# Performance work log

Hardware: AMD Instinct MI355X
Metric: run time of the kernel (lower is better)

Reference implementation:

```python
import jax, jax.numpy as jnp
import numpy as np

N_KERNELS = 5
MUL_FACTOR = 2.0
# 2.0 ** (arange(5) - 2) = [0.25, 0.5, 1, 2, 4]
BANDWIDTH_MULTIPLIERS = MUL_FACTOR ** (np.arange(N_KERNELS) - N_KERNELS // 2)


def setup_inputs() -> dict:
    key = jax.random.key(0)
    kx, ky = jax.random.split(key)
    X = jax.random.normal(kx, (4096, 256), dtype=jnp.float32)
    Y = jax.random.normal(ky, (4096, 256), dtype=jnp.float32)
    return {"X": X, "Y": Y}


def _pairwise_sq_dists(Z):
    # ||z_i - z_j||^2 via GEMM; clamp tiny negatives from roundoff.
    sq = jnp.sum(Z * Z, axis=-1)  # [2N]
    d2 = sq[:, None] + sq[None, :] - 2.0 * (Z @ Z.T)  # [2N, 2N]
    return jnp.maximum(d2, 0.0)


def reference(X, Y):
    n = X.shape[0]
    Z = jnp.concatenate([X, Y], axis=0)  # [2N, D]
    d2 = _pairwise_sq_dists(Z)  # [2N, 2N]
    n_samples = d2.shape[0]
    # bandwidth uses .data in torch -> detached
    bandwidth = jax.lax.stop_gradient(d2.sum()) / (n_samples ** 2 - n_samples)
    mults = jnp.asarray(BANDWIDTH_MULTIPLIERS, dtype=d2.dtype)  # [5]
    # K = sum_k exp(-d2 / (bandwidth * mult_k))
    K = jnp.exp(-d2[None, :, :] / (bandwidth * mults)[:, None, None]).sum(axis=0)
    XX = K[:n, :n].mean()
    XY = K[:n, n:].mean()
    YY = K[n:, n:].mean()
    return XX - 2.0 * XY + YY
```

## Files before the change

### kernel.cpp

```cpp
#include <hip/hip_runtime.h>
#include <math.h>


#define N_HALF 4096
#define DIM 256
#define M_TOT 8192
#define TILE 128
#define NT 64
#define NT_HALF 32
#define CHUNK 4
#define NCHUNK 520

typedef unsigned short ushort_t;
typedef __attribute__((ext_vector_type(8))) short short8;
typedef __attribute__((ext_vector_type(4))) float floatx4;

__device__ ushort_t g_zf[M_TOT * DIM];

__device__ __forceinline__ ushort_t f2bf(float f) {
    unsigned u = __float_as_uint(f);
    u += 0x7fffu + ((u >> 16) & 1u);
    return (ushort_t)(u >> 16);
}

__device__ __forceinline__ void load_frags(const ushort_t* aP, const ushort_t* bP,
                                           int kk, short8 (&af)[4], short8 (&bf)[4]) {
#pragma unroll
    for (int mi = 0; mi < 4; ++mi)
        af[mi] = *(const short8*)(aP + (size_t)mi * 4096 + kk * 512);
#pragma unroll
    for (int ni = 0; ni < 4; ++ni)
        bf[ni] = *(const short8*)(bP + (size_t)ni * 4096 + kk * 512);
}

__device__ __forceinline__ void mfma16(const short8 (&af)[4], const short8 (&bf)[4],
                                       floatx4 (&accv)[4][4]) {
#pragma unroll
    for (int mi = 0; mi < 4; ++mi)
#pragma unroll
        for (int ni = 0; ni < 4; ++ni)
            accv[mi][ni] = __builtin_amdgcn_mfma_f32_16x16x32_bf16(
                af[mi], bf[ni], accv[mi][ni], 0, 0, 0);
}

__global__ __launch_bounds__(256) void k_prep(const float* __restrict__ X,
                                              const float* __restrict__ Y,
                                              float* __restrict__ sq,
                                              float* __restrict__ colsum_r,
                                              float* __restrict__ Ssum_r) {
    __shared__ float cpart[4][256];
    __shared__ float spart[4];
    const int t = threadIdx.x, wave = t >> 6, lane = t & 63;
    const int row0 = blockIdx.x * 16 + wave * 4;
    const int kk = lane >> 3, q = (lane >> 1) & 3, j0 = (lane & 1) * 4;
    float c0 = 0.f, c1 = 0.f, c2 = 0.f, c3 = 0.f, ssum = 0.f;
#pragma unroll
    for (int i = 0; i < 4; ++i) {
        const int row = row0 + i;
        const float* p = (row < N_HALF) ? (X + (size_t)row * DIM)
                                        : (Y + (size_t)(row - N_HALF) * DIM);
        const float4 v = *((const float4*)p + lane);
        ushort4 hi;
        hi.x = f2bf(v.x); hi.y = f2bf(v.y); hi.z = f2bf(v.z); hi.w = f2bf(v.w);
        const int rb = row >> 4, m = row & 15;
        *(ushort4*)(g_zf + (size_t)rb * 4096 + kk * 512 + m * 32 + q * 8 + j0) = hi;
        c0 += v.x; c1 += v.y; c2 += v.z; c3 += v.w;
        float s = fmaf(v.x, v.x, fmaf(v.y, v.y, fmaf(v.z, v.z, v.w * v.w)));
#pragma unroll
        for (int off = 32; off > 0; off >>= 1) s += __shfl_xor(s, off);
        if (lane == 0) sq[row] = s;
        ssum += s;
    }
    float4 cp; cp.x = c0; cp.y = c1; cp.z = c2; cp.w = c3;
    *(float4*)&cpart[wave][lane * 4] = cp;
    if (lane == 0) spart[wave] = ssum;
    __syncthreads();
    const float cs = cpart[0][t] + cpart[1][t] + cpart[2][t] + cpart[3][t];
    const int rep = blockIdx.x & 7;
    atomicAdd(&colsum_r[rep * 256 + t], cs);
    if (t == 0) atomicAdd(&Ssum_r[rep], spart[0] + spart[1] + spart[2] + spart[3]);
}

__global__ __launch_bounds__(256, 2) void k_gram(const float* __restrict__ sq,
                                                 const float* __restrict__ colsum_r,
                                                 const float* __restrict__ Ssum_r,
                                                 double* __restrict__ acc,
                                                 unsigned* __restrict__ cnt,
                                                 float* __restrict__ out) {
    const int bid = (int)blockIdx.x;
    const int cc = (bid & 7) * 65 + (bid >> 3);
    const int f0 = cc * CHUNK;

    __shared__ double redw[4][3];

    const int t = threadIdx.x;
    const int lane = t & 63, wave = t >> 6;
    const int l15 = lane & 15, quad = lane >> 4;
    const int wrow = (wave >> 1) * 64, wcol = (wave & 1) * 64;

    {
        float csf = 0.f;
#pragma unroll
        for (int r = 0; r < 8; ++r) csf += colsum_r[r * 256 + t];
        double p = (double)csf * (double)csf;
#pragma unroll
        for (int off = 32; off > 0; off >>= 1) p += __shfl_xor(p, off);
        if (lane == 0) redw[wave][0] = p;
    }
    __syncthreads();
    const double SS = redw[0][0] + redw[1][0] + redw[2][0] + redw[3][0];
    float Sf = 0.f;
#pragma unroll
    for (int r = 0; r < 8; ++r) Sf += Ssum_r[r];
    const double sum_d2 = 2.0 * (double)M_TOT * (double)Sf - 2.0 * SS;
    const double bw = sum_d2 / ((double)M_TOT * (double)M_TOT - (double)M_TOT);
    const float c2 = (float)(1.4426950408889634 / (4.0 * bw));
    const float twoc2 = 2.f * c2;
    __syncthreads();

    int ti = (int)((129.0f - sqrtf(16641.0f - 8.0f * (float)f0)) * 0.5f);
    if (ti < 0) ti = 0; if (ti > NT - 1) ti = NT - 1;
    while (ti * NT - ti * (ti - 1) / 2 > f0) --ti;
    while ((ti + 1) * NT - (ti + 1) * ti / 2 <= f0) ++ti;
    int tj = ti + (f0 - (ti * NT - ti * (ti - 1) / 2));

    const int laneoff = l15 * 32 + quad * 8;
    const ushort_t* aP = g_zf + (size_t)((ti * TILE + wrow) >> 4) * 4096 + laneoff;
    const ushort_t* bP = g_zf + (size_t)((tj * TILE + wcol) >> 4) * 4096 + laneoff;

    short8 af0[4], bf0[4], af1[4], bf1[4];
    load_frags(aP, bP, 0, af0, bf0);

    double lxx = 0.0, lxy = 0.0, lyy = 0.0;

#pragma unroll 1
    for (int s = 0; s < CHUNK; ++s) {
        floatx4 accv[4][4];
#pragma unroll
        for (int mi = 0; mi < 4; ++mi)
#pragma unroll
            for (int ni = 0; ni < 4; ++ni) accv[mi][ni] = (floatx4)0.f;

#pragma unroll
        for (int kk = 0; kk < 8; kk += 2) {
            load_frags(aP, bP, kk + 1, af1, bf1);
            mfma16(af0, bf0, accv);
            if (kk + 2 < 8) load_frags(aP, bP, kk + 2, af0, bf0);
            mfma16(af1, bf1, accv);
        }

        const int cti = ti, ctj = tj;
        if (s < CHUNK - 1) {
            ++tj; if (tj == NT) { ++ti; tj = ti; }
            aP = g_zf + (size_t)((ti * TILE + wrow) >> 4) * 4096 + laneoff;
            bP = g_zf + (size_t)((tj * TILE + wcol) >> 4) * 4096 + laneoff;
            load_frags(aP, bP, 0, af0, bf0);
        }

        const int arow0 = cti * TILE, brow0 = ctj * TILE;
        float nsj[4];
#pragma unroll
        for (int ni = 0; ni < 4; ++ni)
            nsj[ni] = -c2 * sq[brow0 + wcol + ni * 16 + l15];
        floatx4 nsi4[4];
#pragma unroll
        for (int mi = 0; mi < 4; ++mi) {
            const float4 sv = *(const float4*)&sq[arow0 + wrow + mi * 16 + quad * 4];
            nsi4[mi][0] = -c2 * sv.x; nsi4[mi][1] = -c2 * sv.y;
            nsi4[mi][2] = -c2 * sv.z; nsi4[mi][3] = -c2 * sv.w;
        }
        floatx4 sum4 = (floatx4)0.f;
#pragma unroll
        for (int mi = 0; mi < 4; ++mi) {
#pragma unroll
            for (int ni = 0; ni < 4; ++ni) {
                const floatx4 addv = nsi4[mi] + (floatx4)nsj[ni];
                floatx4 arg = twoc2 * accv[mi][ni] + addv;
                floatx4 tt;
#pragma unroll
                for (int r = 0; r < 4; ++r) tt[r] = exp2f(fminf(arg[r], 0.f));
                const floatx4 t2 = tt * tt, t4 = t2 * t2, t8 = t4 * t4, t16 = t8 * t8;
                sum4 += (tt + t2) + (t4 + t8) + t16;
            }
        }
        const float fsum = (sum4[0] + sum4[1]) + (sum4[2] + sum4[3]);
        const double contrib = ((cti == ctj) ? 1.0 : 2.0) * (double)fsum;
        if (ctj < NT_HALF)       lxx += contrib;
        else if (cti < NT_HALF)  lxy += contrib;
        else                     lyy += contrib;
    }

#pragma unroll
    for (int off = 32; off > 0; off >>= 1) {
        lxx += __shfl_xor(lxx, off);
        lxy += __shfl_xor(lxy, off);
        lyy += __shfl_xor(lyy, off);
    }
    if (lane == 0) { redw[wave][0] = lxx; redw[wave][1] = lxy; redw[wave][2] = lyy; }
    __syncthreads();
    if (t == 0) {
        double sxx = 0.0, sxy = 0.0, syy = 0.0;
#pragma unroll
        for (int wv = 0; wv < 4; ++wv) {
            sxx += redw[wv][0]; sxy += redw[wv][1]; syy += redw[wv][2];
        }
        if (sxx != 0.0) atomicAdd(&acc[0], sxx);
        if (sxy != 0.0) atomicAdd(&acc[1], sxy);
        if (syy != 0.0) atomicAdd(&acc[2], syy);
        __threadfence();
        const unsigned old = atomicAdd(cnt, 1u);
        if (old == (0xAAAAAAAAu + (unsigned)(NCHUNK - 1)) ||
            old == (unsigned)(NCHUNK - 1)) {
            const double xx = atomicAdd(&acc[0], 0.0);
            const double xy = atomicAdd(&acc[1], 0.0);
            const double yy = atomicAdd(&acc[2], 0.0);
            out[0] = (float)((xx + yy - xy) *
                             (1.0 / ((double)N_HALF * (double)N_HALF)));
        }
    }
}

extern "C" void kernel_launch(void* const* d_in, const int* in_sizes, int n_in,
                              void* d_out, int out_size, void* d_ws, size_t ws_size,
                              hipStream_t stream) {
    const float* X = (const float*)d_in[0];
    const float* Y = (const float*)d_in[1];
    char* ws = (char*)d_ws;
    float* sq        = (float*)ws;
    float* colsum_r  = (float*)(ws + 32768);
    float* Ssum_r    = (float*)(ws + 40960);
    unsigned* cnt    = (unsigned*)(ws + 40992);
    double* acc      = (double*)(ws + 41000);
    float* out = (float*)d_out;

    hipLaunchKernelGGL(k_prep, dim3(512), dim3(256), 0, stream,
                       X, Y, sq, colsum_r, Ssum_r);
    hipLaunchKernelGGL(k_gram, dim3(NCHUNK), dim3(256), 0, stream,
                       sq, colsum_r, Ssum_r, acc, cnt, out);
}
```

Before: 136.4 us.

## Use one tile per block and compute bandwidth in a separate kernel

The gram kernel previously gave each of 520 blocks four consecutive upper-triangle tiles. It now launches 2080 blocks with one 128x128 tile each. The per-block bandwidth reduction (colsum squares and Ssum) moves into a new single-block kernel that writes c2 to workspace, so gram blocks only load one float. The aims are finer load balance, more waves in flight to hide latency, and no redundant reduction. The cost is an extra launch, four times as many atomics and counter increments, and the loss of cross-tile fragment prefetch.

```diff
diff --git a/kernel.cpp b/kernel.cpp
--- a/kernel.cpp
+++ b/kernel.cpp
@@ -8,8 +8,7 @@
 #define TILE 128
 #define NT 64
 #define NT_HALF 32
-#define CHUNK 4
-#define NCHUNK 520
+#define NBLK 2080
 
 typedef unsigned short ushort_t;
 typedef __attribute__((ext_vector_type(8))) short short8;
@@ -81,48 +80,53 @@
     if (t == 0) atomicAdd(&Ssum_r[rep], spart[0] + spart[1] + spart[2] + spart[3]);
 }
 
+__global__ __launch_bounds__(256) void k_bw(const float* __restrict__ colsum_r,
+                                            const float* __restrict__ Ssum_r,
+                                            float* __restrict__ c2out) {
+    __shared__ double sred[4];
+    const int t = threadIdx.x, lane = t & 63, wave = t >> 6;
+    float csf = 0.f;
+#pragma unroll
+    for (int r = 0; r < 8; ++r) csf += colsum_r[r * 256 + t];
+    double p = (double)csf * (double)csf;
+#pragma unroll
+    for (int off = 32; off > 0; off >>= 1) p += __shfl_xor(p, off);
+    if (lane == 0) sred[wave] = p;
+    __syncthreads();
+    if (t == 0) {
+        const double SS = sred[0] + sred[1] + sred[2] + sred[3];
+        float Sf = 0.f;
+#pragma unroll
+        for (int r = 0; r < 8; ++r) Sf += Ssum_r[r];
+        const double sum_d2 = 2.0 * (double)M_TOT * (double)Sf - 2.0 * SS;
+        const double bw = sum_d2 / ((double)M_TOT * (double)M_TOT - (double)M_TOT);
+        c2out[0] = (float)(1.4426950408889634 / (4.0 * bw));
+    }
+}
+
 __global__ __launch_bounds__(256, 2) void k_gram(const float* __restrict__ sq,
-                                                 const float* __restrict__ colsum_r,
-                                                 const float* __restrict__ Ssum_r,
+                                                 const float* __restrict__ c2p,
                                                  double* __restrict__ acc,
                                                  unsigned* __restrict__ cnt,
                                                  float* __restrict__ out) {
     const int bid = (int)blockIdx.x;
-    const int cc = (bid & 7) * 65 + (bid >> 3);
-    const int f0 = cc * CHUNK;
-
-    __shared__ double redw[4][3];
+    const int f0 = (bid & 7) * 260 + (bid >> 3);
+
+    __shared__ double redw[4];
 
     const int t = threadIdx.x;
     const int lane = t & 63, wave = t >> 6;
     const int l15 = lane & 15, quad = lane >> 4;
     const int wrow = (wave >> 1) * 64, wcol = (wave & 1) * 64;
 
-    {
-        float csf = 0.f;
-#pragma unroll
-        for (int r = 0; r < 8; ++r) csf += colsum_r[r * 256 + t];
-        double p = (double)csf * (double)csf;
-#pragma unroll
-        for (int off = 32; off > 0; off >>= 1) p += __shfl_xor(p, off);
-        if (lane == 0) redw[wave][0] = p;
-    }
-    __syncthreads();
-    const double SS = redw[0][0] + redw[1][0] + redw[2][0] + redw[3][0];
-    float Sf = 0.f;
-#pragma unroll
-    for (int r = 0; r < 8; ++r) Sf += Ssum_r[r];
-    const double sum_d2 = 2.0 * (double)M_TOT * (double)Sf - 2.0 * SS;
-    const double bw = sum_d2 / ((double)M_TOT * (double)M_TOT - (double)M_TOT);
-    const float c2 = (float)(1.4426950408889634 / (4.0 * bw));
+    const float c2 = c2p[0];
     const float twoc2 = 2.f * c2;
-    __syncthreads();
 
     int ti = (int)((129.0f - sqrtf(16641.0f - 8.0f * (float)f0)) * 0.5f);
     if (ti < 0) ti = 0; if (ti > NT - 1) ti = NT - 1;
     while (ti * NT - ti * (ti - 1) / 2 > f0) --ti;
     while ((ti + 1) * NT - (ti + 1) * ti / 2 <= f0) ++ti;
-    int tj = ti + (f0 - (ti * NT - ti * (ti - 1) / 2));
+    const int tj = ti + (f0 - (ti * NT - ti * (ti - 1) / 2));
 
     const int laneoff = l15 * 32 + quad * 8;
     const ushort_t* aP = g_zf + (size_t)((ti * TILE + wrow) >> 4) * 4096 + laneoff;
@@ -131,86 +135,61 @@
     short8 af0[4], bf0[4], af1[4], bf1[4];
     load_frags(aP, bP, 0, af0, bf0);
 
-    double lxx = 0.0, lxy = 0.0, lyy = 0.0;
-
-#pragma unroll 1
-    for (int s = 0; s < CHUNK; ++s) {
-        floatx4 accv[4][4];
-#pragma unroll
-        for (int mi = 0; mi < 4; ++mi)
-#pragma unroll
-            for (int ni = 0; ni < 4; ++ni) accv[mi][ni] = (floatx4)0.f;
-
-#pragma unroll
-        for (int kk = 0; kk < 8; kk += 2) {
-            load_frags(aP, bP, kk + 1, af1, bf1);
-            mfma16(af0, bf0, accv);
-            if (kk + 2 < 8) load_frags(aP, bP, kk + 2, af0, bf0);
-            mfma16(af1, bf1, accv);
+    floatx4 accv[4][4];
+#pragma unroll
+    for (int mi = 0; mi < 4; ++mi)
+#pragma unroll
+        for (int ni = 0; ni < 4; ++ni) accv[mi][ni] = (floatx4)0.f;
+
+#pragma unroll
+    for (int kk = 0; kk < 8; kk += 2) {
+        load_frags(aP, bP, kk + 1, af1, bf1);
+        mfma16(af0, bf0, accv);
+        if (kk + 2 < 8) load_frags(aP, bP, kk + 2, af0, bf0);
+        mfma16(af1, bf1, accv);
+    }
+
+    const int arow0 = ti * TILE, brow0 = tj * TILE;
+    float nsj[4];
+#pragma unroll
+    for (int ni = 0; ni < 4; ++ni)
+        nsj[ni] = -c2 * sq[brow0 + wcol + ni * 16 + l15];
+    floatx4 nsi4[4];
+#pragma unroll
+    for (int mi = 0; mi < 4; ++mi) {
+        const float4 sv = *(const float4*)&sq[arow0 + wrow + mi * 16 + quad * 4];
+        nsi4[mi][0] = -c2 * sv.x; nsi4[mi][1] = -c2 * sv.y;
+        nsi4[mi][2] = -c2 * sv.z; nsi4[mi][3] = -c2 * sv.w;
+    }
+    floatx4 sum4 = (floatx4)0.f;
+#pragma unroll
+    for (int mi = 0; mi < 4; ++mi) {
+#pragma unroll
+        for (int ni = 0; ni < 4; ++ni) {
+            const floatx4 addv = nsi4[mi] + (floatx4)nsj[ni];
+            floatx4 arg = twoc2 * accv[mi][ni] + addv;
+            floatx4 tt;
+#pragma unroll
+            for (int r = 0; r < 4; ++r) tt[r] = exp2f(fminf(arg[r], 0.f));
+            const floatx4 t2 = tt * tt, t4 = t2 * t2, t8 = t4 * t4, t16 = t8 * t8;
+            sum4 += (tt + t2) + (t4 + t8) + t16;
         }
-
-        const int cti = ti, ctj = tj;
-        if (s < CHUNK - 1) {
-            ++tj; if (tj == NT) { ++ti; tj = ti; }
-            aP = g_zf + (size_t)((ti * TILE + wrow) >> 4) * 4096 + laneoff;
-            bP = g_zf + (size_t)((tj * TILE + wcol) >> 4) * 4096 + laneoff;
-            load_frags(aP, bP, 0, af0, bf0);
-        }
-
-        const int arow0 = cti * TILE, brow0 = ctj * TILE;
-        float nsj[4];
-#pragma unroll
-        for (int ni = 0; ni < 4; ++ni)
-            nsj[ni] = -c2 * sq[brow0 + wcol + ni * 16 + l15];
-        floatx4 nsi4[4];
-#pragma unroll
-        for (int mi = 0; mi < 4; ++mi) {
-            const float4 sv = *(const float4*)&sq[arow0 + wrow + mi * 16 + quad * 4];
-            nsi4[mi][0] = -c2 * sv.x; nsi4[mi][1] = -c2 * sv.y;
-            nsi4[mi][2] = -c2 * sv.z; nsi4[mi][3] = -c2 * sv.w;
-        }
-        floatx4 sum4 = (floatx4)0.f;
-#pragma unroll
-        for (int mi = 0; mi < 4; ++mi) {
-#pragma unroll
-            for (int ni = 0; ni < 4; ++ni) {
-                const floatx4 addv = nsi4[mi] + (floatx4)nsj[ni];
-                floatx4 arg = twoc2 * accv[mi][ni] + addv;
-                floatx4 tt;
-#pragma unroll
-                for (int r = 0; r < 4; ++r) tt[r] = exp2f(fminf(arg[r], 0.f));
-                const floatx4 t2 = tt * tt, t4 = t2 * t2, t8 = t4 * t4, t16 = t8 * t8;
-                sum4 += (tt + t2) + (t4 + t8) + t16;
-            }
-        }
-        const float fsum = (sum4[0] + sum4[1]) + (sum4[2] + sum4[3]);
-        const double contrib = ((cti == ctj) ? 1.0 : 2.0) * (double)fsum;
-        if (ctj < NT_HALF)       lxx += contrib;
-        else if (cti < NT_HALF)  lxy += contrib;
-        else                     lyy += contrib;
-    }
-
-#pragma unroll
-    for (int off = 32; off > 0; off >>= 1) {
-        lxx += __shfl_xor(lxx, off);
-        lxy += __shfl_xor(lxy, off);
-        lyy += __shfl_xor(lyy, off);
-    }
-    if (lane == 0) { redw[wave][0] = lxx; redw[wave][1] = lxy; redw[wave][2] = lyy; }
+    }
+    const float fsum = (sum4[0] + sum4[1]) + (sum4[2] + sum4[3]);
+    double contrib = ((ti == tj) ? 1.0 : 2.0) * (double)fsum;
+
+#pragma unroll
+    for (int off = 32; off > 0; off >>= 1) contrib += __shfl_xor(contrib, off);
+    if (lane == 0) redw[wave] = contrib;
     __syncthreads();
     if (t == 0) {
-        double sxx = 0.0, sxy = 0.0, syy = 0.0;
-#pragma unroll
-        for (int wv = 0; wv < 4; ++wv) {
-            sxx += redw[wv][0]; sxy += redw[wv][1]; syy += redw[wv][2];
-        }
-        if (sxx != 0.0) atomicAdd(&acc[0], sxx);
-        if (sxy != 0.0) atomicAdd(&acc[1], sxy);
-        if (syy != 0.0) atomicAdd(&acc[2], syy);
+        const double s = (redw[0] + redw[1]) + (redw[2] + redw[3]);
+        const int cls = (tj < NT_HALF) ? 0 : ((ti < NT_HALF) ? 1 : 2);
+        if (s != 0.0) atomicAdd(&acc[cls], s);
         __threadfence();
         const unsigned old = atomicAdd(cnt, 1u);
-        if (old == (0xAAAAAAAAu + (unsigned)(NCHUNK - 1)) ||
-            old == (unsigned)(NCHUNK - 1)) {
+        if (old == (0xAAAAAAAAu + (unsigned)(NBLK - 1)) ||
+            old == (unsigned)(NBLK - 1)) {
             const double xx = atomicAdd(&acc[0], 0.0);
             const double xy = atomicAdd(&acc[1], 0.0);
             const double yy = atomicAdd(&acc[2], 0.0);
@@ -231,10 +210,13 @@
     float* Ssum_r    = (float*)(ws + 40960);
     unsigned* cnt    = (unsigned*)(ws + 40992);
     double* acc      = (double*)(ws + 41000);
+    float* c2ws      = (float*)(ws + 41024);
     float* out = (float*)d_out;
 
     hipLaunchKernelGGL(k_prep, dim3(512), dim3(256), 0, stream,
                        X, Y, sq, colsum_r, Ssum_r);
-    hipLaunchKernelGGL(k_gram, dim3(NCHUNK), dim3(256), 0, stream,
-                       sq, colsum_r, Ssum_r, acc, cnt, out);
-}
+    hipLaunchKernelGGL(k_bw, dim3(1), dim3(256), 0, stream,
+                       colsum_r, Ssum_r, c2ws);
+    hipLaunchKernelGGL(k_gram, dim3(NBLK), dim3(256), 0, stream,
+                       sq, c2ws, acc, cnt, out);
+}
```

Measured after the change: 145.1 us. +6.4%, slower.

## Stage Gram tiles through double-buffered LDS and hoist bandwidth into separate kernel

Applied to the files above, without the earlier changes.

Each k_gram block now stages its A and B tile slices into a double-buffered LDS region with global_load_lds, instead of having every wave read its MFMA fragments straight from global memory. Staging overlaps with the MFMA work on the other buffer and lets waves that share rows or columns reuse the same data. The bandwidth reduction, previously repeated in every block, moves into a tiny single-block k_bw kernel that writes c2 to workspace. The cost is a __syncthreads per k-slice, 32KB of LDS per block, and one extra kernel launch.

```diff
diff --git a/kernel.cpp b/kernel.cpp
--- a/kernel.cpp
+++ b/kernel.cpp
@@ -23,18 +23,33 @@
     return (ushort_t)(u >> 16);
 }
 
-__device__ __forceinline__ void load_frags(const ushort_t* aP, const ushort_t* bP,
-                                           int kk, short8 (&af)[4], short8 (&bf)[4]) {
+__device__ __forceinline__ void gload_lds16(const ushort_t* g, ushort_t* l) {
+    __builtin_amdgcn_global_load_lds(
+        (const __attribute__((address_space(1))) void*)g,
+        (__attribute__((address_space(3))) void*)l, 16, 0, 0);
+}
+
+__device__ __forceinline__ void stage_slice(const ushort_t* gA, const ushort_t* gB,
+                                            ushort_t* lA, ushort_t* lB,
+                                            int wave, int lane) {
+#pragma unroll
+    for (int i = 0; i < 2; ++i) {
+        const int c = wave * 2 + i;
+        gload_lds16(gA + (size_t)c * 4096 + lane * 8, lA + c * 512);
+        gload_lds16(gB + (size_t)c * 4096 + lane * 8, lB + c * 512);
+    }
+}
+
+__device__ __forceinline__ void compute_kk(const ushort_t* lA, const ushort_t* lB,
+                                           int a0, int b0, int laneoff,
+                                           floatx4 (&accv)[4][4]) {
+    short8 af[4], bf[4];
 #pragma unroll
     for (int mi = 0; mi < 4; ++mi)
-        af[mi] = *(const short8*)(aP + (size_t)mi * 4096 + kk * 512);
+        af[mi] = *(const short8*)(lA + (a0 + mi) * 512 + laneoff);
 #pragma unroll
     for (int ni = 0; ni < 4; ++ni)
-        bf[ni] = *(const short8*)(bP + (size_t)ni * 4096 + kk * 512);
-}
-
-__device__ __forceinline__ void mfma16(const short8 (&af)[4], const short8 (&bf)[4],
-                                       floatx4 (&accv)[4][4]) {
+        bf[ni] = *(const short8*)(lB + (b0 + ni) * 512 + laneoff);
 #pragma unroll
     for (int mi = 0; mi < 4; ++mi)
 #pragma unroll
@@ -81,42 +96,51 @@
     if (t == 0) atomicAdd(&Ssum_r[rep], spart[0] + spart[1] + spart[2] + spart[3]);
 }
 
+__global__ __launch_bounds__(256) void k_bw(const float* __restrict__ colsum_r,
+                                            const float* __restrict__ Ssum_r,
+                                            float* __restrict__ c2out) {
+    __shared__ double sred[4];
+    const int t = threadIdx.x, lane = t & 63, wave = t >> 6;
+    float csf = 0.f;
+#pragma unroll
+    for (int r = 0; r < 8; ++r) csf += colsum_r[r * 256 + t];
+    double p = (double)csf * (double)csf;
+#pragma unroll
+    for (int off = 32; off > 0; off >>= 1) p += __shfl_xor(p, off);
+    if (lane == 0) sred[wave] = p;
+    __syncthreads();
+    if (t == 0) {
+        const double SS = sred[0] + sred[1] + sred[2] + sred[3];
+        float Sf = 0.f;
+#pragma unroll
+        for (int r = 0; r < 8; ++r) Sf += Ssum_r[r];
+        const double sum_d2 = 2.0 * (double)M_TOT * (double)Sf - 2.0 * SS;
+        const double bw = sum_d2 / ((double)M_TOT * (double)M_TOT - (double)M_TOT);
+        c2out[0] = (float)(1.4426950408889634 / (4.0 * bw));
+    }
+}
+
 __global__ __launch_bounds__(256, 2) void k_gram(const float* __restrict__ sq,
-                                                 const float* __restrict__ colsum_r,
-                                                 const float* __restrict__ Ssum_r,
+                                                 const float* __restrict__ c2p,
                                                  double* __restrict__ acc,
                                                  unsigned* __restrict__ cnt,
                                                  float* __restrict__ out) {
+    __shared__ __attribute__((aligned(16))) ushort_t lds[2][8192];
+    __shared__ double redw[4][3];
+
     const int bid = (int)blockIdx.x;
     const int cc = (bid & 7) * 65 + (bid >> 3);
     const int f0 = cc * CHUNK;
-
-    __shared__ double redw[4][3];
 
     const int t = threadIdx.x;
     const int lane = t & 63, wave = t >> 6;
     const int l15 = lane & 15, quad = lane >> 4;
     const int wrow = (wave >> 1) * 64, wcol = (wave & 1) * 64;
-
-    {
-        float csf = 0.f;
-#pragma unroll
-        for (int r = 0; r < 8; ++r) csf += colsum_r[r * 256 + t];
-        double p = (double)csf * (double)csf;
-#pragma unroll
-        for (int off = 32; off > 0; off >>= 1) p += __shfl_xor(p, off);
-        if (lane == 0) redw[wave][0] = p;
-    }
-    __syncthreads();
-    const double SS = redw[0][0] + redw[1][0] + redw[2][0] + redw[3][0];
-    float Sf = 0.f;
-#pragma unroll
-    for (int r = 0; r < 8; ++r) Sf += Ssum_r[r];
-    const double sum_d2 = 2.0 * (double)M_TOT * (double)Sf - 2.0 * SS;
-    const double bw = sum_d2 / ((double)M_TOT * (double)M_TOT - (double)M_TOT);
-    const float c2 = (float)(1.4426950408889634 / (4.0 * bw));
+    const int a0 = (wave >> 1) * 4, b0 = (wave & 1) * 4;
+    const int laneoff = l15 * 32 + quad * 8;
+
+    const float c2 = c2p[0];
     const float twoc2 = 2.f * c2;
-    __syncthreads();
 
     int ti = (int)((129.0f - sqrtf(16641.0f - 8.0f * (float)f0)) * 0.5f);
     if (ti < 0) ti = 0; if (ti > NT - 1) ti = NT - 1;
@@ -124,17 +148,22 @@
     while ((ti + 1) * NT - (ti + 1) * ti / 2 <= f0) ++ti;
     int tj = ti + (f0 - (ti * NT - ti * (ti - 1) / 2));
 
-    const int laneoff = l15 * 32 + quad * 8;
-    const ushort_t* aP = g_zf + (size_t)((ti * TILE + wrow) >> 4) * 4096 + laneoff;
-    const ushort_t* bP = g_zf + (size_t)((tj * TILE + wcol) >> 4) * 4096 + laneoff;
-
-    short8 af0[4], bf0[4], af1[4], bf1[4];
-    load_frags(aP, bP, 0, af0, bf0);
+    const ushort_t* cgA = g_zf + (size_t)ti * 8 * 4096;
+    const ushort_t* cgB = g_zf + (size_t)tj * 8 * 4096;
+
+    stage_slice(cgA, cgB, lds[0], lds[0] + 4096, wave, lane);
+    __syncthreads();
 
     double lxx = 0.0, lxy = 0.0, lyy = 0.0;
+    int cur = 0;
 
 #pragma unroll 1
     for (int s = 0; s < CHUNK; ++s) {
+        int nti = ti, ntj = tj + 1;
+        if (ntj == NT) { ++nti; ntj = nti; }
+        const ushort_t* ngA = g_zf + (size_t)nti * 8 * 4096;
+        const ushort_t* ngB = g_zf + (size_t)ntj * 8 * 4096;
+
         floatx4 accv[4][4];
 #pragma unroll
         for (int mi = 0; mi < 4; ++mi)
@@ -142,22 +171,19 @@
             for (int ni = 0; ni < 4; ++ni) accv[mi][ni] = (floatx4)0.f;
 
 #pragma unroll
-        for (int kk = 0; kk < 8; kk += 2) {
-            load_frags(aP, bP, kk + 1, af1, bf1);
-            mfma16(af0, bf0, accv);
-            if (kk + 2 < 8) load_frags(aP, bP, kk + 2, af0, bf0);
-            mfma16(af1, bf1, accv);
-        }
-
-        const int cti = ti, ctj = tj;
-        if (s < CHUNK - 1) {
-            ++tj; if (tj == NT) { ++ti; tj = ti; }
-            aP = g_zf + (size_t)((ti * TILE + wrow) >> 4) * 4096 + laneoff;
-            bP = g_zf + (size_t)((tj * TILE + wcol) >> 4) * 4096 + laneoff;
-            load_frags(aP, bP, 0, af0, bf0);
-        }
-
-        const int arow0 = cti * TILE, brow0 = ctj * TILE;
+        for (int kk = 0; kk < 8; ++kk) {
+            if (kk < 7)
+                stage_slice(cgA + (kk + 1) * 512, cgB + (kk + 1) * 512,
+                            lds[cur ^ 1], lds[cur ^ 1] + 4096, wave, lane);
+            else if (s < CHUNK - 1)
+                stage_slice(ngA, ngB,
+                            lds[cur ^ 1], lds[cur ^ 1] + 4096, wave, lane);
+            compute_kk(lds[cur], lds[cur] + 4096, a0, b0, laneoff, accv);
+            __syncthreads();
+            cur ^= 1;
+        }
+
+        const int arow0 = ti * TILE, brow0 = tj * TILE;
         float nsj[4];
 #pragma unroll
         for (int ni = 0; ni < 4; ++ni)
@@ -184,10 +210,12 @@
             }
         }
         const float fsum = (sum4[0] + sum4[1]) + (sum4[2] + sum4[3]);
-        const double contrib = ((cti == ctj) ? 1.0 : 2.0) * (double)fsum;
-        if (ctj < NT_HALF)       lxx += contrib;
-        else if (cti < NT_HALF)  lxy += contrib;
-        else                     lyy += contrib;
+        const double contrib = ((ti == tj) ? 1.0 : 2.0) * (double)fsum;
+        if (tj < NT_HALF)       lxx += contrib;
+        else if (ti < NT_HALF)  lxy += contrib;
+        else                    lyy += contrib;
+
+        ti = nti; tj = ntj; cgA = ngA; cgB = ngB;
     }
 
 #pragma unroll
@@ -231,10 +259,13 @@
     float* Ssum_r    = (float*)(ws + 40960);
     unsigned* cnt    = (unsigned*)(ws + 40992);
     double* acc      = (double*)(ws + 41000);
+    float* c2ws      = (float*)(ws + 41024);
     float* out = (float*)d_out;
 
     hipLaunchKernelGGL(k_prep, dim3(512), dim3(256), 0, stream,
                        X, Y, sq, colsum_r, Ssum_r);
+    hipLaunchKernelGGL(k_bw, dim3(1), dim3(256), 0, stream,
+                       colsum_r, Ssum_r, c2ws);
     hipLaunchKernelGGL(k_gram, dim3(NCHUNK), dim3(256), 0, stream,
-                       sq, colsum_r, Ssum_r, acc, cnt, out);
-}
+                       sq, c2ws, acc, cnt, out);
+}
```

Measured after the change: 117.7 us. 13.7% less time.
